# Kernel tuning notes

Hardware: AMD Instinct MI355X
Metric: run time of the kernel (lower is better)

## Reference

```python
import jax, jax.numpy as jnp
import numpy as np

B, D_IN, R, D_P, K, D_C, ITERS = 4096, 2048, 7, 128, 25, 16, 3


def _ln(x, g, b, eps=1e-5):
    m = jnp.mean(x, axis=-1, keepdims=True)
    v = jnp.var(x, axis=-1, keepdims=True)
    return (x - m) * jax.lax.rsqrt(v + eps) * g + b


def _squash(x):
    eps = 1e-6
    ns = jnp.sum(x * x, axis=-1, keepdims=True)
    scale = ns / jnp.maximum(1.0 + ns, eps)
    return scale * x / (jnp.sqrt(ns) + eps)


def setup_inputs() -> dict:
    key = jax.random.key(0)
    ks = jax.random.split(key, 8)
    f = lambda k, shp, s=0.02: (jax.random.normal(k, shp) * s).astype(jnp.float32)
    return {
        "z": jax.random.normal(ks[0], (B, D_IN), jnp.float32),
        "W_prim": f(ks[1], (D_IN, R * D_P)),
        "b_prim": jnp.zeros((R * D_P,), jnp.float32),
        "ln_a_g": jnp.ones((D_IN,), jnp.float32),
        "ln_a_b": jnp.zeros((D_IN,), jnp.float32),
        "W_act": f(ks[2], (D_IN, R)),
        "b_act": jnp.zeros((R,), jnp.float32),
        "w_caps": (np.sqrt(K / (D_P * R)).astype(np.float32)
                   * jax.random.normal(ks[3], (R, D_P, K, D_C))).astype(jnp.float32),
        "ln_c_g": jnp.ones((D_C,), jnp.float32),
        "ln_c_b": jnp.zeros((D_C,), jnp.float32),
        "beta_u": f(ks[4], (K,), 1.0),
        "ln_h_g": jnp.ones((R * D_C,), jnp.float32),
        "ln_h_b": jnp.zeros((R * D_C,), jnp.float32),
        "W_h1": f(ks[5], (R * D_C, 4 * R * D_C)),
        "b_h1": jnp.zeros((4 * R * D_C,), jnp.float32),
        "W_h2": f(ks[6], (4 * R * D_C, 1)),
        "b_h2": jnp.zeros((1,), jnp.float32),
    }


def reference(z, W_prim, b_prim, ln_a_g, ln_a_b, W_act, b_act, w_caps,
              ln_c_g, ln_c_b, beta_u, ln_h_g, ln_h_b, W_h1, b_h1, W_h2, b_h2):
    # primary capsules: [B, R, D_P] poses + [B, R] activations
    pose = _squash((z @ W_prim + b_prim).reshape(B, R, D_P))
    act = jnp.clip(jax.nn.sigmoid(_ln(z, ln_a_g, ln_a_b) @ W_act + b_act), 0.0, 1.0)

    # votes: [B, R, K, D_C]
    u = jnp.einsum('brd,rdkh->brkh', pose, w_caps)
    scale = 1.0 / np.sqrt(D_C).astype(np.float32)

    # iterative routing (EM/softmax-agreement style)
    q = jnp.full((B, R, K), 1.0 / K, dtype=z.dtype)
    class_pose = None
    for _ in range(ITERS):
        wts = q * act[:, :, None]                               # [B,R,K]
        class_pose = _ln(jnp.einsum('brk,brkh->bkh', wts, u), ln_c_g, ln_c_b)
        agree = jnp.einsum('bkh,brkh->brk', class_pose, u) * scale
        q = jax.nn.softmax(agree, axis=-1)

    class_act = jax.nn.sigmoid(beta_u[None, :] + jnp.einsum('brk,br->bk', q, act))
    route_class_emb = q[..., None] * u                          # [B,R,K,D_C]

    # concat per-route interaction vectors -> [B, K, R*D_C]
    class_embed = jnp.transpose(route_class_emb, (0, 2, 1, 3)).reshape(B, K, R * D_C)
    h = jax.nn.gelu(_ln(class_embed, ln_h_g, ln_h_b) @ W_h1 + b_h1, approximate=False)
    logits = (h @ W_h2 + b_h2)[..., 0]                          # [B, K]

    return (logits, class_embed, class_pose, class_act, q, pose, act, route_class_emb)
```

## Files before the change

### kernel.cpp

```cpp
#include <hip/hip_runtime.h>
#include <cstddef>

#define BB 4096
#define DIN 2048
#define RR 7
#define DP 128
#define KK 25
#define DC 16
#define NITERS 3
#define RKH (RR*KK*DC)
#define RK  (RR*KK)
#define KH  (KK*DC)
#define HD  (RR*DC)
#define H4  (4*HD)
#define HEAD_TILES (BB*KK/128)

typedef __attribute__((ext_vector_type(8))) short bf16x8;
typedef __attribute__((ext_vector_type(4))) float f32x4;

__device__ __forceinline__ unsigned pk_bf16(float a, float b) {
    union { float f; unsigned u; } xa, xb;
    xa.f = a; xb.f = b;
    unsigned ua = (xa.u + 0x7FFFu + ((xa.u >> 16) & 1u)) >> 16;
    unsigned ub = (xb.u + 0x7FFFu + ((xb.u >> 16) & 1u)) >> 16;
    return (ua & 0xFFFFu) | (ub << 16);
}

__device__ __forceinline__ float gelu_tanh(float x) {
    float x3 = x * x * x;
    float tt = 0.7978845608f * (x + 0.044715f * x3);
    float e = __expf(2.0f * tt);
    float th = 1.0f - 2.0f / (e + 1.0f);
    return 0.5f * x * (1.0f + th);
}

__device__ __forceinline__ float gelu_fast(float x) {
    float u = x * __builtin_fmaf(x * x, 0.07135655f, 1.5957691f);
    u = fmaxf(u, -30.0f);
    float e = __expf(-u);
    return x * __builtin_amdgcn_rcpf(1.0f + e);
}

__global__ __launch_bounds__(256) void transpose_cvt_kernel(
    const float* __restrict__ src, unsigned short* __restrict__ dst, int RS, int CS)
{
    __shared__ float T[64][65];
    int r0 = blockIdx.x * 64, c0 = blockIdx.y * 64;
    size_t bo = (size_t)blockIdx.z * RS * CS;
    src += bo; dst += bo;
    int t = threadIdx.x;
    for (int s = t; s < 64 * 16; s += 256) {
        int row = s >> 4, c4 = s & 15;
        int gr = r0 + row, gc = c0 + c4 * 4;
        float4 v = make_float4(0.f, 0.f, 0.f, 0.f);
        if (gr < RS && gc < CS) v = *(const float4*)(src + (size_t)gr * CS + gc);
        T[row][c4 * 4 + 0] = v.x; T[row][c4 * 4 + 1] = v.y;
        T[row][c4 * 4 + 2] = v.z; T[row][c4 * 4 + 3] = v.w;
    }
    __syncthreads();
    for (int s = t; s < 64 * 16; s += 256) {
        int col = s >> 4, r4 = s & 15;
        int gc = c0 + col, gr = r0 + r4 * 4;
        if (gc < CS && gr + 3 < RS) {
            unsigned lo = pk_bf16(T[r4 * 4 + 0][col], T[r4 * 4 + 1][col]);
            unsigned hi = pk_bf16(T[r4 * 4 + 2][col], T[r4 * 4 + 3][col]);
            *(uint2*)(dst + (size_t)gc * RS + gr) = make_uint2(lo, hi);
        }
    }
}

__global__ __launch_bounds__(256) void w1_frag_kernel(
    const float* __restrict__ W1, unsigned short* __restrict__ W1F)
{
    int d = blockIdx.x * 256 + threadIdx.x;
    int e2 = d & 3;
    int lane = (d >> 2) & 63;
    int fid = d >> 8;
    int j = fid & 3, ks = (fid >> 2) & 3, nc = fid >> 4;
    int col = nc * 64 + j * 16 + (lane & 15);
    int k = ks * 32 + (lane >> 4) * 8 + e2 * 2;
    float a = (k < HD)     ? W1[(size_t)k * H4 + col]       : 0.f;
    float b = (k + 1 < HD) ? W1[(size_t)(k + 1) * H4 + col] : 0.f;
    ((unsigned*)W1F)[d] = pk_bf16(a, b);
}

__global__ __launch_bounds__(256) void act_kernel(
    const float* __restrict__ z, const float* __restrict__ g, const float* __restrict__ bb,
    const float* __restrict__ Wa, const float* __restrict__ ba,
    float* __restrict__ act_out)
{
    int b = blockIdx.x;
    int t = threadIdx.x;
    __shared__ float zs[DIN];
    __shared__ float ws1[4], ws2[4];
    __shared__ float wr[4][RR];
    const float* zr = z + (size_t)b * DIN;
    float s = 0.f, s2 = 0.f;
    for (int i = t; i < DIN; i += 256) {
        float v = zr[i]; zs[i] = v; s += v; s2 += v * v;
    }
    for (int off = 32; off; off >>= 1) { s += __shfl_down(s, off); s2 += __shfl_down(s2, off); }
    int w = t >> 6, lane = t & 63;
    if (lane == 0) { ws1[w] = s; ws2[w] = s2; }
    __syncthreads();
    s  = ws1[0] + ws1[1] + ws1[2] + ws1[3];
    s2 = ws2[0] + ws2[1] + ws2[2] + ws2[3];
    float mean = s * (1.0f / DIN);
    float var  = s2 * (1.0f / DIN) - mean * mean;
    float rstd = rsqrtf(var + 1e-5f);
    float acc[RR];
#pragma unroll
    for (int r = 0; r < RR; ++r) acc[r] = 0.f;
    for (int i = t; i < DIN; i += 256) {
        float y = (zs[i] - mean) * rstd * g[i] + bb[i];
#pragma unroll
        for (int r = 0; r < RR; ++r) acc[r] += y * Wa[i * RR + r];
    }
    for (int off = 32; off; off >>= 1) {
#pragma unroll
        for (int r = 0; r < RR; ++r) acc[r] += __shfl_down(acc[r], off);
    }
    if (lane == 0) {
#pragma unroll
        for (int r = 0; r < RR; ++r) wr[w][r] = acc[r];
    }
    __syncthreads();
    if (t < RR) {
        float v = wr[0][t] + wr[1][t] + wr[2][t] + wr[3][t] + ba[t];
        float sg = 1.0f / (1.0f + expf(-v));
        sg = fminf(fmaxf(sg, 0.0f), 1.0f);
        act_out[(size_t)b * RR + t] = sg;
    }
}

__global__ __launch_bounds__(256) void pose_mfma(
    const float* __restrict__ z, const unsigned short* __restrict__ WpT,
    const float* __restrict__ bp, float* __restrict__ pose_out)
{
    __shared__ __align__(16) unsigned short As[128 * 40];
    __shared__ __align__(16) unsigned short Bs[128 * 40];
    __shared__ float sq[2][128];
    int m0 = blockIdx.x * 128, r = blockIdx.y, t = threadIdx.x;
    int n0 = r * DP;
    int w = t >> 6, l = t & 63;
    int lrow = l & 15, koff = l >> 4;
    int rbase = (w >> 1) * 64, cbase = (w & 1) * 64;
    f32x4 acc[4][4];
#pragma unroll
    for (int i = 0; i < 4; ++i)
#pragma unroll
        for (int j = 0; j < 4; ++j) acc[i][j] = 0.0f;
    for (int kt = 0; kt < DIN; kt += 32) {
#pragma unroll
        for (int q = 0; q < 4; ++q) {
            int s = t + 256 * q;
            int row = s >> 3, k4 = s & 7;
            float4 v = *(const float4*)(z + (size_t)(m0 + row) * DIN + kt + k4 * 4);
            *(uint2*)(As + row * 40 + k4 * 4) = make_uint2(pk_bf16(v.x, v.y), pk_bf16(v.z, v.w));
        }
#pragma unroll
        for (int q = 0; q < 2; ++q) {
            int s = t + 256 * q;
            int col = s >> 2, k8 = s & 3;
            uint4 v = *(const uint4*)(WpT + (size_t)(n0 + col) * DIN + kt + k8 * 8);
            *(uint4*)(Bs + col * 40 + k8 * 8) = v;
        }
        __syncthreads();
        bf16x8 a[4], b[4];
#pragma unroll
        for (int i = 0; i < 4; ++i)
            a[i] = *(const bf16x8*)(As + (rbase + i * 16 + lrow) * 40 + koff * 8);
#pragma unroll
        for (int j = 0; j < 4; ++j)
            b[j] = *(const bf16x8*)(Bs + (cbase + j * 16 + lrow) * 40 + koff * 8);
#pragma unroll
        for (int i = 0; i < 4; ++i)
#pragma unroll
            for (int j = 0; j < 4; ++j)
                acc[i][j] = __builtin_amdgcn_mfma_f32_16x16x32_bf16(a[i], b[j], acc[i][j], 0, 0, 0);
        __syncthreads();
    }
    float bpv[4];
#pragma unroll
    for (int j = 0; j < 4; ++j) bpv[j] = bp[n0 + cbase + j * 16 + lrow];
    float ns_[4][4];
#pragma unroll
    for (int i = 0; i < 4; ++i)
#pragma unroll
        for (int reg = 0; reg < 4; ++reg) {
            float ss = 0.f;
#pragma unroll
            for (int j = 0; j < 4; ++j) {
                float x = acc[i][j][reg] + bpv[j];
                acc[i][j][reg] = x;
                ss += x * x;
            }
            ss += __shfl_xor(ss, 1); ss += __shfl_xor(ss, 2);
            ss += __shfl_xor(ss, 4); ss += __shfl_xor(ss, 8);
            ns_[i][reg] = ss;
        }
    if (lrow == 0) {
#pragma unroll
        for (int i = 0; i < 4; ++i)
#pragma unroll
            for (int reg = 0; reg < 4; ++reg)
                sq[w & 1][rbase + i * 16 + koff * 4 + reg] = ns_[i][reg];
    }
    __syncthreads();
#pragma unroll
    for (int i = 0; i < 4; ++i)
#pragma unroll
        for (int reg = 0; reg < 4; ++reg) {
            int rl = rbase + i * 16 + koff * 4 + reg;
            float ns = sq[0][rl] + sq[1][rl];
            float factor = (ns / fmaxf(1.0f + ns, 1e-6f)) / (sqrtf(ns) + 1e-6f);
            size_t rowbase = ((size_t)(m0 + rl) * RR + r) * DP;
#pragma unroll
            for (int j = 0; j < 4; ++j)
                pose_out[rowbase + cbase + j * 16 + lrow] = acc[i][j][reg] * factor;
        }
}

__global__ __launch_bounds__(256) void votes_mfma(
    const float* __restrict__ pose, const unsigned short* __restrict__ wcT,
    float* __restrict__ u_out)
{
    __shared__ __align__(16) unsigned short As[128 * 152];
    __shared__ __align__(16) unsigned short Bs[80 * 152];
    int m0 = blockIdx.x * 128, r = blockIdx.y, n0 = blockIdx.z * 80;
    int t = threadIdx.x;
    int w = t >> 6, l = t & 63;
    int lrow = l & 15, koff = l >> 4;
    int rbase = w * 32;
#pragma unroll
    for (int q = 0; q < 16; ++q) {
        int s = t + 256 * q;
        int row = s >> 5, k4 = s & 31;
        float4 v = *(const float4*)(pose + ((size_t)(m0 + row) * RR + r) * DP + k4 * 4);
        *(uint2*)(As + row * 152 + k4 * 4) = make_uint2(pk_bf16(v.x, v.y), pk_bf16(v.z, v.w));
    }
    const unsigned short* wr_ = wcT + (size_t)r * KH * DP;
#pragma unroll
    for (int q = 0; q < 5; ++q) {
        int s = t + 256 * q;
        int col = s >> 4, k8 = s & 15;
        uint4 v = *(const uint4*)(wr_ + (size_t)(n0 + col) * DP + k8 * 8);
        *(uint4*)(Bs + col * 152 + k8 * 8) = v;
    }
    __syncthreads();
    f32x4 acc[2][5];
#pragma unroll
    for (int i = 0; i < 2; ++i)
#pragma unroll
        for (int j = 0; j < 5; ++j) acc[i][j] = 0.0f;
#pragma unroll
    for (int ks = 0; ks < 4; ++ks) {
        bf16x8 a[2], b[5];
#pragma unroll
        for (int i = 0; i < 2; ++i)
            a[i] = *(const bf16x8*)(As + (rbase + i * 16 + lrow) * 152 + ks * 32 + koff * 8);
#pragma unroll
        for (int j = 0; j < 5; ++j)
            b[j] = *(const bf16x8*)(Bs + (j * 16 + lrow) * 152 + ks * 32 + koff * 8);
#pragma unroll
        for (int i = 0; i < 2; ++i)
#pragma unroll
            for (int j = 0; j < 5; ++j)
                acc[i][j] = __builtin_amdgcn_mfma_f32_16x16x32_bf16(a[i], b[j], acc[i][j], 0, 0, 0);
    }
#pragma unroll
    for (int i = 0; i < 2; ++i)
#pragma unroll
        for (int reg = 0; reg < 4; ++reg) {
            int row = m0 + rbase + i * 16 + koff * 4 + reg;
            size_t base = ((size_t)row * RR + r) * KH + n0;
#pragma unroll
            for (int j = 0; j < 5; ++j)
                u_out[base + j * 16 + lrow] = acc[i][j][reg];
        }
}

__global__ __launch_bounds__(64) void routing_kernel(
    const float* __restrict__ u_in, const float* __restrict__ act_in,
    const float* __restrict__ lncg, const float* __restrict__ lncb,
    const float* __restrict__ beta_u,
    float* __restrict__ q_out, float* __restrict__ cp_out,
    float* __restrict__ ca_out, float* __restrict__ rce_out,
    float* __restrict__ ce_out)
{
    __shared__ __align__(16) float U[RKH];
    __shared__ float Q[RK];
    __shared__ float CP[KH];
    __shared__ float AG[RK];
    __shared__ float A7[RR];
    int b = blockIdx.x, t = threadIdx.x;
    const float4* u4 = (const float4*)(u_in + (size_t)b * RKH);
    float4* U4 = (float4*)U;
    for (int p = t; p < RKH / 4; p += 64) U4[p] = u4[p];
    if (t < RR) A7[t] = act_in[(size_t)b * RR + t];
    for (int p = t; p < RK; p += 64) Q[p] = 1.0f / KK;
    __syncthreads();
    for (int it = 0; it < NITERS; ++it) {
        for (int p = t; p < KH; p += 64) {
            int k = p / DC;
            float s = 0.f;
#pragma unroll
            for (int r = 0; r < RR; ++r) s += Q[r * KK + k] * A7[r] * U[r * KH + p];
            CP[p] = s;
        }
        __syncthreads();
        if (t < KK) {
            float m = 0.f;
#pragma unroll
            for (int h = 0; h < DC; ++h) m += CP[t * DC + h];
            m *= (1.0f / DC);
            float v = 0.f;
#pragma unroll
            for (int h = 0; h < DC; ++h) { float d = CP[t * DC + h] - m; v += d * d; }
            v *= (1.0f / DC);
            float rstd = rsqrtf(v + 1e-5f);
#pragma unroll
            for (int h = 0; h < DC; ++h)
                CP[t * DC + h] = (CP[t * DC + h] - m) * rstd * lncg[h] + lncb[h];
        }
        __syncthreads();
        for (int p = t; p < RK; p += 64) {
            int r = p / KK, k = p % KK;
            float s = 0.f;
#pragma unroll
            for (int h = 0; h < DC; ++h) s += CP[k * DC + h] * U[r * KH + k * DC + h];
            AG[p] = s * 0.25f;
        }
        __syncthreads();
        if (t < RR) {
            float mx = -1e30f;
            for (int k = 0; k < KK; ++k) mx = fmaxf(mx, AG[t * KK + k]);
            float e[KK], sum = 0.f;
            for (int k = 0; k < KK; ++k) { e[k] = expf(AG[t * KK + k] - mx); sum += e[k]; }
            float inv = 1.0f / sum;
            for (int k = 0; k < KK; ++k) Q[t * KK + k] = e[k] * inv;
        }
        __syncthreads();
    }
    if (t < KK) {
        float s = 0.f;
#pragma unroll
        for (int r = 0; r < RR; ++r) s += Q[r * KK + t] * A7[r];
        ca_out[(size_t)b * KK + t] = 1.0f / (1.0f + expf(-(beta_u[t] + s)));
    }
    for (int p = t; p < RK; p += 64) q_out[(size_t)b * RK + p] = Q[p];
    for (int p = t; p < KH; p += 64) cp_out[(size_t)b * KH + p] = CP[p];
    float4* rce4 = (float4*)(rce_out + (size_t)b * RKH);
    float4* ce4  = (float4*)ce_out;
    for (int p4 = t; p4 < RKH / 4; p4 += 64) {
        int base = p4 * 4;
        int r  = base / KH;
        int k  = (base % KH) / DC;
        int h0 = base % DC;
        float qv = Q[r * KK + k];
        float4 uv = U4[p4];
        float4 rv = make_float4(qv * uv.x, qv * uv.y, qv * uv.z, qv * uv.w);
        rce4[p4] = rv;
        size_t ci = ((size_t)b * RKH + (size_t)k * HD + (size_t)r * DC + h0) >> 2;
        ce4[ci] = rv;
    }
}

__global__ __launch_bounds__(512) void head_mfma(
    const float* __restrict__ ce, const float* __restrict__ g, const float* __restrict__ bb,
    const unsigned short* __restrict__ W1F, const float* __restrict__ b1,
    const float* __restrict__ W2, const float* __restrict__ b2,
    float* __restrict__ logits)
{
    __shared__ __align__(16) unsigned short As[128 * 128];
    __shared__ __align__(16) unsigned short Bs[448 * 128];
    __shared__ float LB1[H4];
    __shared__ float LW2[H4];
    int t = threadIdx.x;
    int w = t >> 6, l = t & 63;
    int lrow = l & 15, koff = l >> 4;

#pragma unroll
    for (int q = 0; q < 14; ++q) {
        int chunk = w * 14 + q;
        __builtin_amdgcn_global_load_lds(
            (const __attribute__((address_space(1))) unsigned int*)(const void*)(W1F + (size_t)chunk * 512 + l * 8),
            (__attribute__((address_space(3))) unsigned int*)(void*)(Bs + chunk * 512),
            16, 0, 0);
    }
    if (t >= 256) {
        for (int s = t - 256; s < H4; s += 256) { LB1[s] = b1[s]; LW2[s] = W2[s]; }
    }
    float b2v = b2[0];

    int row = t >> 1, half = t & 1;
    int lr = row & 15, rt = row >> 4;

    float4 v[14];
    int tile = blockIdx.x;
    if (t < 256 && tile < HEAD_TILES) {
        const float* rp = ce + (size_t)(tile * 128 + row) * HD + half * 56;
#pragma unroll
        for (int m = 0; m < 14; ++m) v[m] = *(const float4*)(rp + m * 4);
    }

    bool first = true;
    for (; tile < HEAD_TILES; tile += 256) {
        if (!first) __syncthreads();
        first = false;

        if (t < 256) {
            float s1 = 0.f, s2 = 0.f;
#pragma unroll
            for (int m = 0; m < 14; ++m) {
                s1 += v[m].x + v[m].y + v[m].z + v[m].w;
                s2 += v[m].x * v[m].x + v[m].y * v[m].y + v[m].z * v[m].z + v[m].w * v[m].w;
            }
            s1 += __shfl_xor(s1, 1); s2 += __shfl_xor(s2, 1);
            float mean = s1 * (1.0f / HD);
            float var  = s2 * (1.0f / HD) - mean * mean;
            float rstd = rsqrtf(var + 1e-5f);
#pragma unroll
            for (int j = 0; j < 7; ++j) {
                float4 gl0 = *(const float4*)(g  + half * 56 + j * 8);
                float4 gl1 = *(const float4*)(g  + half * 56 + j * 8 + 4);
                float4 bl0 = *(const float4*)(bb + half * 56 + j * 8);
                float4 bl1 = *(const float4*)(bb + half * 56 + j * 8 + 4);
                float4 x0 = v[j * 2], x1 = v[j * 2 + 1];
                float y0 = (x0.x - mean) * rstd * gl0.x + bl0.x;
                float y1 = (x0.y - mean) * rstd * gl0.y + bl0.y;
                float y2 = (x0.z - mean) * rstd * gl0.z + bl0.z;
                float y3 = (x0.w - mean) * rstd * gl0.w + bl0.w;
                float y4 = (x1.x - mean) * rstd * gl1.x + bl1.x;
                float y5 = (x1.y - mean) * rstd * gl1.y + bl1.y;
                float y6 = (x1.z - mean) * rstd * gl1.z + bl1.z;
                float y7 = (x1.w - mean) * rstd * gl1.w + bl1.w;
                int k8 = half * 7 + j;
                int ks = k8 >> 2, ko = k8 & 3;
                unsigned* dst = (unsigned*)(As + (size_t)((rt * 4 + ks) * 64 + ko * 16 + lr) * 8);
                dst[0] = pk_bf16(y0, y1); dst[1] = pk_bf16(y2, y3);
                dst[2] = pk_bf16(y4, y5); dst[3] = pk_bf16(y6, y7);
            }
            if (half) {
                uint4 z4 = make_uint4(0, 0, 0, 0);
                *(uint4*)(As + (size_t)((rt * 4 + 3) * 64 + 2 * 16 + lr) * 8) = z4;
                *(uint4*)(As + (size_t)((rt * 4 + 3) * 64 + 3 * 16 + lr) * 8) = z4;
            }
        }
        __syncthreads();

        bf16x8 af[4];
#pragma unroll
        for (int ks = 0; ks < 4; ++ks)
            af[ks] = *(const bf16x8*)(As + (size_t)((w * 4 + ks) * 64 + l) * 8);

        if (t < 256 && tile + 256 < HEAD_TILES) {
            const float* rp = ce + (size_t)((tile + 256) * 128 + row) * HD + half * 56;
#pragma unroll
            for (int m = 0; m < 14; ++m) v[m] = *(const float4*)(rp + m * 4);
        }

        float logitAcc[4];
#pragma unroll
        for (int reg = 0; reg < 4; ++reg) logitAcc[reg] = 0.f;

        for (int nc = 0; nc < 7; ++nc) {
            float b1v[4], w2v[4];
#pragma unroll
            for (int j = 0; j < 4; ++j) {
                b1v[j] = LB1[nc * 64 + j * 16 + lrow];
                w2v[j] = LW2[nc * 64 + j * 16 + lrow];
            }
            f32x4 acc[4];
#pragma unroll
            for (int j = 0; j < 4; ++j) acc[j] = 0.0f;
#pragma unroll
            for (int ks = 0; ks < 4; ++ks) {
                bf16x8 bfr[4];
#pragma unroll
                for (int j = 0; j < 4; ++j)
                    bfr[j] = *(const bf16x8*)(Bs + (size_t)(((nc * 4 + ks) * 4 + j) * 64 + l) * 8);
#pragma unroll
                for (int j = 0; j < 4; ++j)
                    acc[j] = __builtin_amdgcn_mfma_f32_16x16x32_bf16(af[ks], bfr[j], acc[j], 0, 0, 0);
            }
#pragma unroll
            for (int reg = 0; reg < 4; ++reg) {
                float sum = 0.f;
#pragma unroll
                for (int j = 0; j < 4; ++j) {
                    float x = acc[j][reg] + b1v[j];
                    sum += gelu_fast(x) * w2v[j];
                }
                logitAcc[reg] += sum;
            }
        }
#pragma unroll
        for (int reg = 0; reg < 4; ++reg) {
            float vv = logitAcc[reg];
            vv += __shfl_xor(vv, 1); vv += __shfl_xor(vv, 2);
            vv += __shfl_xor(vv, 4); vv += __shfl_xor(vv, 8);
            if (lrow == 0)
                logits[(size_t)tile * 128 + w * 16 + koff * 4 + reg] = vv + b2v;
        }
    }
}

__global__ __launch_bounds__(256) void pose_kernel(
    const float* __restrict__ z, const float* __restrict__ Wp, const float* __restrict__ bp,
    float* __restrict__ pose_out)
{
    __shared__ __align__(16) float As[64 * 36];
    __shared__ __align__(16) float Bs[32 * 128];
    int m0 = blockIdx.x * 64;
    int r  = blockIdx.y;
    int n0 = r * DP;
    int t  = threadIdx.x;
    int rg = t >> 5;
    int cg = t & 31;
    float acc[8][4] = {};
    for (int kt = 0; kt < DIN; kt += 32) {
#pragma unroll
        for (int q = 0; q < 2; ++q) {
            int s = t * 2 + q;
            int row = s >> 3, k4 = s & 7;
            float4 v = *(const float4*)(z + (size_t)(m0 + row) * DIN + kt + k4 * 4);
            *(float4*)(As + row * 36 + k4 * 4) = v;
        }
#pragma unroll
        for (int q = 0; q < 4; ++q) {
            int s = t + 256 * q;
            int row = s >> 5, c4 = s & 31;
            float4 v = *(const float4*)(Wp + (size_t)(kt + row) * (RR * DP) + n0 + c4 * 4);
            *(float4*)(Bs + row * 128 + c4 * 4) = v;
        }
        __syncthreads();
#pragma unroll
        for (int kk = 0; kk < 32; ++kk) {
            float4 bv = *(const float4*)(Bs + kk * 128 + cg * 4);
#pragma unroll
            for (int j = 0; j < 8; ++j) {
                float a = As[(rg * 8 + j) * 36 + kk];
                acc[j][0] += a * bv.x; acc[j][1] += a * bv.y;
                acc[j][2] += a * bv.z; acc[j][3] += a * bv.w;
            }
        }
        __syncthreads();
    }
    float bi0 = bp[n0 + cg * 4], bi1 = bp[n0 + cg * 4 + 1];
    float bi2 = bp[n0 + cg * 4 + 2], bi3 = bp[n0 + cg * 4 + 3];
#pragma unroll
    for (int j = 0; j < 8; ++j) {
        float x0 = acc[j][0] + bi0, x1 = acc[j][1] + bi1;
        float x2 = acc[j][2] + bi2, x3 = acc[j][3] + bi3;
        float ns = x0 * x0 + x1 * x1 + x2 * x2 + x3 * x3;
        for (int off = 1; off < 32; off <<= 1) ns += __shfl_xor(ns, off);
        float factor = (ns / fmaxf(1.0f + ns, 1e-6f)) / (sqrtf(ns) + 1e-6f);
        int row = m0 + rg * 8 + j;
        float4 o = make_float4(x0 * factor, x1 * factor, x2 * factor, x3 * factor);
        *(float4*)(pose_out + ((size_t)row * RR + r) * DP + cg * 4) = o;
    }
}

__global__ __launch_bounds__(256) void votes_kernel(
    const float* __restrict__ pose, const float* __restrict__ wc,
    float* __restrict__ u_out)
{
    __shared__ float As[64 * 129];
    __shared__ __align__(16) float Bs[64 * 80];
    int m0 = blockIdx.x * 64;
    int r  = blockIdx.y;
    int n0 = blockIdx.z * 80;
    int t  = threadIdx.x;
    const size_t wbase = (size_t)r * DP * KH;
#pragma unroll
    for (int q = 0; q < 8; ++q) {
        int s = t + 256 * q;
        int row = s >> 5, d4 = s & 31;
        float4 v = *(const float4*)(pose + ((size_t)(m0 + row) * RR + r) * DP + d4 * 4);
        As[row * 129 + d4 * 4 + 0] = v.x;
        As[row * 129 + d4 * 4 + 1] = v.y;
        As[row * 129 + d4 * 4 + 2] = v.z;
        As[row * 129 + d4 * 4 + 3] = v.w;
    }
    int m4 = t >> 4, n5 = t & 15;
    float acc[4][5];
#pragma unroll
    for (int i = 0; i < 4; ++i)
#pragma unroll
        for (int j = 0; j < 5; ++j) acc[i][j] = 0.f;
    for (int kt = 0; kt < DP; kt += 64) {
        __syncthreads();
#pragma unroll
        for (int q = 0; q < 5; ++q) {
            int s = t + 256 * q;
            int d = s / 20, c4 = s % 20;
            float4 v = *(const float4*)(wc + wbase + (size_t)(kt + d) * KH + n0 + c4 * 4);
            *(float4*)(Bs + d * 80 + c4 * 4) = v;
        }
        __syncthreads();
#pragma unroll 4
        for (int dd = 0; dd < 64; ++dd) {
            int d = kt + dd;
            float b_[5];
#pragma unroll
            for (int j = 0; j < 5; ++j) b_[j] = Bs[dd * 80 + n5 * 5 + j];
#pragma unroll
            for (int i = 0; i < 4; ++i) {
                float a = As[(m4 * 4 + i) * 129 + d];
#pragma unroll
                for (int j = 0; j < 5; ++j) acc[i][j] += a * b_[j];
            }
        }
    }
#pragma unroll
    for (int i = 0; i < 4; ++i) {
        int row = m0 + m4 * 4 + i;
        size_t base = ((size_t)row * RR + r) * KH + n0 + n5 * 5;
#pragma unroll
        for (int j = 0; j < 5; ++j) u_out[base + j] = acc[i][j];
    }
}

__global__ __launch_bounds__(256) void head_kernel(
    const float* __restrict__ ce, const float* __restrict__ g, const float* __restrict__ bb,
    const float* __restrict__ W1, const float* __restrict__ b1,
    const float* __restrict__ W2, const float* __restrict__ b2,
    float* __restrict__ logits)
{
    __shared__ __align__(16) float Y[64 * HD];
    __shared__ float Wc[HD * 64];
    __shared__ float Lg[64];
    int row0 = blockIdx.x * 64;
    int t = threadIdx.x;
    for (int s = t; s < 64 * HD; s += 256) Y[s] = ce[(size_t)row0 * HD + s];
    __syncthreads();
    if (t < 64) {
        float m = 0.f;
        for (int i = 0; i < HD; ++i) m += Y[t * HD + i];
        m *= (1.0f / HD);
        float v = 0.f;
        for (int i = 0; i < HD; ++i) { float d = Y[t * HD + i] - m; v += d * d; }
        v *= (1.0f / HD);
        float rstd = rsqrtf(v + 1e-5f);
        for (int i = 0; i < HD; ++i) Y[t * HD + i] = (Y[t * HD + i] - m) * rstd * g[i] + bb[i];
    }
    int rg = t >> 4;
    int cg = t & 15;
    float accRow[4] = {0.f, 0.f, 0.f, 0.f};
    for (int c0 = 0; c0 < H4; c0 += 64) {
        __syncthreads();
        for (int s = t; s < HD * 64; s += 256) {
            int i = s >> 6, c = s & 63;
            Wc[i * 64 + c] = W1[(size_t)i * H4 + c0 + c];
        }
        __syncthreads();
        float b1v[4], w2v[4];
#pragma unroll
        for (int c = 0; c < 4; ++c) { b1v[c] = b1[c0 + cg * 4 + c]; w2v[c] = W2[c0 + cg * 4 + c]; }
        float s_[4][4];
#pragma unroll
        for (int rr = 0; rr < 4; ++rr)
#pragma unroll
            for (int c = 0; c < 4; ++c) s_[rr][c] = b1v[c];
        for (int i4 = 0; i4 < HD / 4; ++i4) {
            float4 y4[4];
#pragma unroll
            for (int rr = 0; rr < 4; ++rr)
                y4[rr] = *(const float4*)(Y + (rg * 4 + rr) * HD + i4 * 4);
#pragma unroll
            for (int is = 0; is < 4; ++is) {
                float w_[4];
#pragma unroll
                for (int c = 0; c < 4; ++c) w_[c] = Wc[(i4 * 4 + is) * 64 + cg * 4 + c];
#pragma unroll
                for (int rr = 0; rr < 4; ++rr) {
                    float yv = (is == 0) ? y4[rr].x : (is == 1) ? y4[rr].y : (is == 2) ? y4[rr].z : y4[rr].w;
#pragma unroll
                    for (int c = 0; c < 4; ++c) s_[rr][c] += yv * w_[c];
                }
            }
        }
#pragma unroll
        for (int rr = 0; rr < 4; ++rr) {
#pragma unroll
            for (int c = 0; c < 4; ++c) {
                float x = s_[rr][c];
                float ge = 0.5f * x * (1.0f + erff(x * 0.70710678118654752440f));
                accRow[rr] += ge * w2v[c];
            }
        }
    }
#pragma unroll
    for (int rr = 0; rr < 4; ++rr) {
        float v = accRow[rr];
        v += __shfl_xor(v, 1); v += __shfl_xor(v, 2);
        v += __shfl_xor(v, 4); v += __shfl_xor(v, 8);
        if (cg == 0) Lg[rg * 4 + rr] = v;
    }
    __syncthreads();
    if (t < 64) logits[row0 + t] = Lg[t] + b2[0];
}

extern "C" void kernel_launch(void* const* d_in, const int* in_sizes, int n_in,
                              void* d_out, int out_size, void* d_ws, size_t ws_size,
                              hipStream_t stream) {
    const float* z    = (const float*)d_in[0];
    const float* Wp   = (const float*)d_in[1];
    const float* bp   = (const float*)d_in[2];
    const float* lnag = (const float*)d_in[3];
    const float* lnab = (const float*)d_in[4];
    const float* Wa   = (const float*)d_in[5];
    const float* ba   = (const float*)d_in[6];
    const float* wc   = (const float*)d_in[7];
    const float* lncg = (const float*)d_in[8];
    const float* lncb = (const float*)d_in[9];
    const float* beta = (const float*)d_in[10];
    const float* lnhg = (const float*)d_in[11];
    const float* lnhb = (const float*)d_in[12];
    const float* W1   = (const float*)d_in[13];
    const float* b1   = (const float*)d_in[14];
    const float* W2   = (const float*)d_in[15];
    const float* b2   = (const float*)d_in[16];

    float* out = (float*)d_out;
    float* o_logits = out;
    float* o_ce   = o_logits + (size_t)BB * KK;
    float* o_cp   = o_ce   + (size_t)BB * KK * HD;
    float* o_ca   = o_cp   + (size_t)BB * KK * DC;
    float* o_q    = o_ca   + (size_t)BB * KK;
    float* o_pose = o_q    + (size_t)BB * RK;
    float* o_act  = o_pose + (size_t)BB * RR * DP;
    float* o_rce  = o_act  + (size_t)BB * RR;

    const size_t WPT_ELE = (size_t)(RR * DP) * DIN;
    const size_t W1F_ELE = (size_t)H4 * 128;
    const size_t WCT_ELE = (size_t)RR * KH * DP;
    const size_t WS_NEED = (WPT_ELE + W1F_ELE + WCT_ELE) * sizeof(unsigned short);
    unsigned short* WpT = (unsigned short*)d_ws;
    unsigned short* W1F = WpT + WPT_ELE;
    unsigned short* wcT = W1F + W1F_ELE;

    hipLaunchKernelGGL(act_kernel, dim3(BB), dim3(256), 0, stream,
                       z, lnag, lnab, Wa, ba, o_act);

    if (ws_size >= WS_NEED) {
        hipLaunchKernelGGL(transpose_cvt_kernel, dim3(DIN / 64, (RR * DP) / 64, 1), dim3(256), 0, stream,
                           Wp, WpT, DIN, RR * DP);
        hipLaunchKernelGGL(w1_frag_kernel, dim3(112), dim3(256), 0, stream,
                           W1, W1F);
        hipLaunchKernelGGL(transpose_cvt_kernel, dim3(2, 7, RR), dim3(256), 0, stream,
                           wc, wcT, DP, KH);
        hipLaunchKernelGGL(pose_mfma, dim3(BB / 128, RR), dim3(256), 0, stream,
                           z, WpT, bp, o_pose);
        hipLaunchKernelGGL(votes_mfma, dim3(BB / 128, RR, 5), dim3(256), 0, stream,
                           o_pose, wcT, o_rce);
        hipLaunchKernelGGL(routing_kernel, dim3(BB), dim3(64), 0, stream,
                           o_rce, o_act, lncg, lncb, beta, o_q, o_cp, o_ca, o_rce, o_ce);
        hipLaunchKernelGGL(head_mfma, dim3(256), dim3(512), 0, stream,
                           o_ce, lnhg, lnhb, W1F, b1, W2, b2, o_logits);
    } else {
        hipLaunchKernelGGL(pose_kernel, dim3(BB / 64, RR), dim3(256), 0, stream,
                           z, Wp, bp, o_pose);
        hipLaunchKernelGGL(votes_kernel, dim3(BB / 64, RR, 5), dim3(256), 0, stream,
                           o_pose, wc, o_rce);
        hipLaunchKernelGGL(routing_kernel, dim3(BB), dim3(64), 0, stream,
                           o_rce, o_act, lncg, lncb, beta, o_q, o_cp, o_ca, o_rce, o_ce);
        hipLaunchKernelGGL(head_kernel, dim3(BB * KK / 64), dim3(256), 0, stream,
                           o_ce, lnhg, lnhb, W1, b1, W2, b2, o_logits);
    }
}
```

Baseline: 351.9 us.

## Pre-pack z and W_prim into MFMA fragment layout and pipeline pose GEMM

The act kernel now also writes z as bf16 in an MFMA-fragment-tiled layout, and a new kernel packs W_prim the same way. A new pose GEMM with 512 threads then streams both operands straight into LDS with global_load_lds under double buffering, replacing the older kernel that converted z on the fly and staged through registers. The aim is to cut the pose GEMM's load and conversion overhead and overlap loads with MFMA work. In exchange it needs more workspace and writes an extra bf16 copy of z. The old path is kept as a fallback when workspace is too small.

```diff
diff --git a/kernel.cpp b/kernel.cpp
--- a/kernel.cpp
+++ b/kernel.cpp
@@ -26,14 +26,6 @@
     return (ua & 0xFFFFu) | (ub << 16);
 }
 
-__device__ __forceinline__ float gelu_tanh(float x) {
-    float x3 = x * x * x;
-    float tt = 0.7978845608f * (x + 0.044715f * x3);
-    float e = __expf(2.0f * tt);
-    float th = 1.0f - 2.0f / (e + 1.0f);
-    return 0.5f * x * (1.0f + th);
-}
-
 __device__ __forceinline__ float gelu_fast(float x) {
     float u = x * __builtin_fmaf(x * x, 0.07135655f, 1.5957691f);
     u = fmaxf(u, -30.0f);
@@ -84,10 +76,35 @@
     ((unsigned*)W1F)[d] = pk_bf16(a, b);
 }
 
+__global__ __launch_bounds__(256) void wpf_kernel(
+    const float* __restrict__ Wp, unsigned short* __restrict__ wpf)
+{
+    int tid = blockIdx.x * 256 + threadIdx.x;
+    int lane = tid & 63;
+    int CH = tid >> 6;
+    int c = CH & 63, gcol = CH >> 6;
+    int n = gcol * 16 + (lane & 15);
+    int k0 = c * 32 + (lane >> 4) * 8;
+    unsigned d0, d1, d2, d3;
+    {
+        float a0 = Wp[(size_t)(k0 + 0) * (RR * DP) + n];
+        float a1 = Wp[(size_t)(k0 + 1) * (RR * DP) + n];
+        float a2 = Wp[(size_t)(k0 + 2) * (RR * DP) + n];
+        float a3 = Wp[(size_t)(k0 + 3) * (RR * DP) + n];
+        float a4 = Wp[(size_t)(k0 + 4) * (RR * DP) + n];
+        float a5 = Wp[(size_t)(k0 + 5) * (RR * DP) + n];
+        float a6 = Wp[(size_t)(k0 + 6) * (RR * DP) + n];
+        float a7 = Wp[(size_t)(k0 + 7) * (RR * DP) + n];
+        d0 = pk_bf16(a0, a1); d1 = pk_bf16(a2, a3);
+        d2 = pk_bf16(a4, a5); d3 = pk_bf16(a6, a7);
+    }
+    *(uint4*)(wpf + (size_t)tid * 8) = make_uint4(d0, d1, d2, d3);
+}
+
 __global__ __launch_bounds__(256) void act_kernel(
     const float* __restrict__ z, const float* __restrict__ g, const float* __restrict__ bb,
     const float* __restrict__ Wa, const float* __restrict__ ba,
-    float* __restrict__ act_out)
+    float* __restrict__ act_out, unsigned short* __restrict__ zf_out)
 {
     int b = blockIdx.x;
     int t = threadIdx.x;
@@ -103,6 +120,16 @@
     int w = t >> 6, lane = t & 63;
     if (lane == 0) { ws1[w] = s; ws2[w] = s2; }
     __syncthreads();
+    if (zf_out) {
+        int c = t >> 2, o = t & 3;
+        const float* zp = zs + c * 32 + o * 8;
+        unsigned d0 = pk_bf16(zp[0], zp[1]);
+        unsigned d1 = pk_bf16(zp[2], zp[3]);
+        unsigned d2 = pk_bf16(zp[4], zp[5]);
+        unsigned d3 = pk_bf16(zp[6], zp[7]);
+        size_t off2 = (((size_t)(b >> 4) * 64 + c) * 64 + (size_t)(o * 16 + (b & 15))) * 8;
+        *(uint4*)(zf_out + off2) = make_uint4(d0, d1, d2, d3);
+    }
     s  = ws1[0] + ws1[1] + ws1[2] + ws1[3];
     s2 = ws2[0] + ws2[1] + ws2[2] + ws2[3];
     float mean = s * (1.0f / DIN);
@@ -131,6 +158,107 @@
         sg = fminf(fmaxf(sg, 0.0f), 1.0f);
         act_out[(size_t)b * RR + t] = sg;
     }
+}
+
+#define POSE_STAGE(KS, BUF) do {                                                            \
+    _Pragma("unroll")                                                                       \
+    for (int q = 0; q < 4; ++q) {                                                           \
+        int ch = w * 4 + q;                                                                 \
+        int gi = ch >> 2, cc = ch & 3;                                                      \
+        __builtin_amdgcn_global_load_lds(                                                   \
+            (const __attribute__((address_space(1))) unsigned int*)(const void*)            \
+                (zf + (((size_t)(zbase + gi) * 64) + (KS) * 4 + cc) * 512 + l * 8),         \
+            (__attribute__((address_space(3))) unsigned int*)(void*)                        \
+                (&As[BUF][ch * 512 + l * 8]), 16, 0, 0);                                    \
+        __builtin_amdgcn_global_load_lds(                                                   \
+            (const __attribute__((address_space(1))) unsigned int*)(const void*)            \
+                (wpf + (((size_t)(wbase + gi) * 64) + (KS) * 4 + cc) * 512 + l * 8),        \
+            (__attribute__((address_space(3))) unsigned int*)(void*)                        \
+                (&Bs[BUF][ch * 512 + l * 8]), 16, 0, 0);                                    \
+    }                                                                                       \
+} while (0)
+
+__global__ __launch_bounds__(512) void pose_mfma2(
+    const unsigned short* __restrict__ zf, const unsigned short* __restrict__ wpf,
+    const float* __restrict__ bp, float* __restrict__ pose_out)
+{
+    __shared__ __align__(16) unsigned short As[2][32 * 512];
+    __shared__ __align__(16) unsigned short Bs[2][32 * 512];
+    __shared__ float sq[2][128];
+    int m0 = blockIdx.x * 128, r = blockIdx.y;
+    int t = threadIdx.x, w = t >> 6, l = t & 63;
+    int wr = w >> 1, wc = w & 1;
+    int lrow = l & 15, koff = l >> 4;
+    int zbase = m0 >> 4;
+    int wbase = r * 8;
+
+    f32x4 acc[2][4];
+#pragma unroll
+    for (int i = 0; i < 2; ++i)
+#pragma unroll
+        for (int j = 0; j < 4; ++j) acc[i][j] = 0.0f;
+
+    POSE_STAGE(0, 0);
+    __syncthreads();
+    for (int ks = 0; ks < 16; ++ks) {
+        int cur = ks & 1;
+        if (ks < 15) POSE_STAGE(ks + 1, cur ^ 1);
+#pragma unroll
+        for (int c = 0; c < 4; ++c) {
+            bf16x8 a[2], b[4];
+#pragma unroll
+            for (int i = 0; i < 2; ++i)
+                a[i] = *(const bf16x8*)(&As[cur][((wr * 2 + i) * 4 + c) * 512 + l * 8]);
+#pragma unroll
+            for (int j = 0; j < 4; ++j)
+                b[j] = *(const bf16x8*)(&Bs[cur][((wc * 4 + j) * 4 + c) * 512 + l * 8]);
+#pragma unroll
+            for (int i = 0; i < 2; ++i)
+#pragma unroll
+                for (int j = 0; j < 4; ++j)
+                    acc[i][j] = __builtin_amdgcn_mfma_f32_16x16x32_bf16(a[i], b[j], acc[i][j], 0, 0, 0);
+        }
+        __syncthreads();
+    }
+    float bpv[4];
+#pragma unroll
+    for (int j = 0; j < 4; ++j) bpv[j] = bp[r * DP + wc * 64 + j * 16 + lrow];
+    float ns_[2][4];
+#pragma unroll
+    for (int i = 0; i < 2; ++i)
+#pragma unroll
+        for (int reg = 0; reg < 4; ++reg) {
+            float ss = 0.f;
+#pragma unroll
+            for (int j = 0; j < 4; ++j) {
+                float x = acc[i][j][reg] + bpv[j];
+                acc[i][j][reg] = x;
+                ss += x * x;
+            }
+            ss += __shfl_xor(ss, 1); ss += __shfl_xor(ss, 2);
+            ss += __shfl_xor(ss, 4); ss += __shfl_xor(ss, 8);
+            ns_[i][reg] = ss;
+        }
+    if (lrow == 0) {
+#pragma unroll
+        for (int i = 0; i < 2; ++i)
+#pragma unroll
+            for (int reg = 0; reg < 4; ++reg)
+                sq[wc][wr * 32 + i * 16 + koff * 4 + reg] = ns_[i][reg];
+    }
+    __syncthreads();
+#pragma unroll
+    for (int i = 0; i < 2; ++i)
+#pragma unroll
+        for (int reg = 0; reg < 4; ++reg) {
+            int rl = wr * 32 + i * 16 + koff * 4 + reg;
+            float ns = sq[0][rl] + sq[1][rl];
+            float factor = (ns / fmaxf(1.0f + ns, 1e-6f)) / (sqrtf(ns) + 1e-6f);
+            size_t rowbase = ((size_t)(m0 + rl) * RR + r) * DP;
+#pragma unroll
+            for (int j = 0; j < 4; ++j)
+                pose_out[rowbase + wc * 64 + j * 16 + lrow] = acc[i][j][reg] * factor;
+        }
 }
 
 __global__ __launch_bounds__(256) void pose_mfma(
@@ -733,22 +861,41 @@
     float* o_act  = o_pose + (size_t)BB * RR * DP;
     float* o_rce  = o_act  + (size_t)BB * RR;
 
-    const size_t WPT_ELE = (size_t)(RR * DP) * DIN;
     const size_t W1F_ELE = (size_t)H4 * 128;
     const size_t WCT_ELE = (size_t)RR * KH * DP;
-    const size_t WS_NEED = (WPT_ELE + W1F_ELE + WCT_ELE) * sizeof(unsigned short);
-    unsigned short* WpT = (unsigned short*)d_ws;
-    unsigned short* W1F = WpT + WPT_ELE;
+    const size_t ZF_ELE  = (size_t)BB * DIN;
+    const size_t WPF_ELE = (size_t)(RR * DP) * DIN;
+    const size_t WPT_ELE = WPF_ELE;
+    unsigned short* W1F = (unsigned short*)d_ws;
     unsigned short* wcT = W1F + W1F_ELE;
-
-    hipLaunchKernelGGL(act_kernel, dim3(BB), dim3(256), 0, stream,
-                       z, lnag, lnab, Wa, ba, o_act);
-
-    if (ws_size >= WS_NEED) {
+    unsigned short* zf  = wcT + WCT_ELE;
+    unsigned short* wpf = zf + ZF_ELE;
+    unsigned short* WpT = zf;
+
+    const size_t WS_NEW = (W1F_ELE + WCT_ELE + ZF_ELE + WPF_ELE) * sizeof(unsigned short);
+    const size_t WS_MID = (W1F_ELE + WCT_ELE + WPT_ELE) * sizeof(unsigned short);
+
+    if (ws_size >= WS_NEW) {
+        hipLaunchKernelGGL(act_kernel, dim3(BB), dim3(256), 0, stream,
+                           z, lnag, lnab, Wa, ba, o_act, zf);
+        hipLaunchKernelGGL(wpf_kernel, dim3(896), dim3(256), 0, stream, Wp, wpf);
+        hipLaunchKernelGGL(w1_frag_kernel, dim3(112), dim3(256), 0, stream, W1, W1F);
+        hipLaunchKernelGGL(transpose_cvt_kernel, dim3(2, 7, RR), dim3(256), 0, stream,
+                           wc, wcT, DP, KH);
+        hipLaunchKernelGGL(pose_mfma2, dim3(BB / 128, RR), dim3(512), 0, stream,
+                           zf, wpf, bp, o_pose);
+        hipLaunchKernelGGL(votes_mfma, dim3(BB / 128, RR, 5), dim3(256), 0, stream,
+                           o_pose, wcT, o_rce);
+        hipLaunchKernelGGL(routing_kernel, dim3(BB), dim3(64), 0, stream,
+                           o_rce, o_act, lncg, lncb, beta, o_q, o_cp, o_ca, o_rce, o_ce);
+        hipLaunchKernelGGL(head_mfma, dim3(256), dim3(512), 0, stream,
+                           o_ce, lnhg, lnhb, W1F, b1, W2, b2, o_logits);
+    } else if (ws_size >= WS_MID) {
+        hipLaunchKernelGGL(act_kernel, dim3(BB), dim3(256), 0, stream,
+                           z, lnag, lnab, Wa, ba, o_act, (unsigned short*)nullptr);
         hipLaunchKernelGGL(transpose_cvt_kernel, dim3(DIN / 64, (RR * DP) / 64, 1), dim3(256), 0, stream,
                            Wp, WpT, DIN, RR * DP);
-        hipLaunchKernelGGL(w1_frag_kernel, dim3(112), dim3(256), 0, stream,
-                           W1, W1F);
+        hipLaunchKernelGGL(w1_frag_kernel, dim3(112), dim3(256), 0, stream, W1, W1F);
         hipLaunchKernelGGL(transpose_cvt_kernel, dim3(2, 7, RR), dim3(256), 0, stream,
                            wc, wcT, DP, KH);
         hipLaunchKernelGGL(pose_mfma, dim3(BB / 128, RR), dim3(256), 0, stream,
@@ -760,6 +907,8 @@
         hipLaunchKernelGGL(head_mfma, dim3(256), dim3(512), 0, stream,
                            o_ce, lnhg, lnhb, W1F, b1, W2, b2, o_logits);
     } else {
+        hipLaunchKernelGGL(act_kernel, dim3(BB), dim3(256), 0, stream,
+                           z, lnag, lnab, Wa, ba, o_act, (unsigned short*)nullptr);
         hipLaunchKernelGGL(pose_kernel, dim3(BB / 64, RR), dim3(256), 0, stream,
                            z, Wp, bp, o_pose);
         hipLaunchKernelGGL(votes_kernel, dim3(BB / 64, RR, 5), dim3(256), 0, stream,
```

Result: faster. 326.8 us (-7.1%).
